# Optimization experiments

Measured on AMD Instinct MI355X. Metric: run time of the kernel, lower is better.

Reference implementation:

```python
import jax, jax.numpy as jnp
import numpy as np

NUM_HEADS = 16

def _stablemax3_s(x):
    # 3rd-order Taylor approx of exp(x), Eq 38
    pos = 1.0 + x * (1.0 + 0.5 * x * (1.0 + x / 3.0))
    neg = 1.0 / (1.0 - x * (1.0 - 0.5 * x * (1.0 - x / 3.0)))
    return jnp.where(x >= 0, pos, neg)

def stablemax3(logits, axis=-1):
    logits = logits - jnp.max(logits, axis=axis, keepdims=True)
    s = _stablemax3_s(logits)
    return s / jnp.sum(s, axis=axis, keepdims=True)

def setup_inputs() -> dict:
    key = jax.random.key(0)
    k1, k2, k3 = jax.random.split(key, 3)
    B, S, D = 2, 2048, 1024
    x = jax.random.normal(k1, (B, S, D), dtype=jnp.float32)
    w_qkv = jax.random.normal(k2, (3 * D, D), dtype=jnp.float32) * 0.02
    w_out = jax.random.normal(k3, (D, D), dtype=jnp.float32) * 0.02
    b_out = jnp.zeros((D,), dtype=jnp.float32)
    return {"x": x, "w_qkv": w_qkv, "w_out": w_out, "b_out": b_out}

def reference(x, w_qkv, w_out, b_out):
    B, S, D = x.shape
    H = NUM_HEADS
    hd = D // H
    scale = hd ** (-0.5)
    qkv = x @ w_qkv.T                                  # [B, S, 3D]
    qkv = qkv.reshape(B, S, 3, H, hd)
    qkv = jnp.transpose(qkv, (2, 0, 3, 1, 4))          # [3, B, H, S, hd]
    q, k, v = qkv[0], qkv[1], qkv[2]                   # pos(.) is identity here
    attn = jnp.einsum('bhsd,bhtd->bhst', q, k) * scale # [B, H, S, S]
    attn = stablemax3(attn, axis=-1)
    out = jnp.einsum('bhst,bhtd->bhsd', attn, v)       # [B, H, S, hd]
    out = jnp.transpose(out, (0, 2, 1, 3)).reshape(B, S, D)
    return out @ w_out.T + b_out
```

## Files before the change

### kernel.cpp

```cpp
#include <hip/hip_runtime.h>

typedef _Float16 half8 __attribute__((ext_vector_type(8)));
typedef _Float16 half4 __attribute__((ext_vector_type(4)));
typedef _Float16 half2v __attribute__((ext_vector_type(2)));
typedef float floatx4 __attribute__((ext_vector_type(4)));

__device__ __forceinline__ void gl_lds16(const _Float16* g, _Float16* l) {
    __builtin_amdgcn_global_load_lds(
        (const __attribute__((address_space(1))) void*)g,
        (__attribute__((address_space(3))) void*)l, 16, 0, 0);
}

__device__ __forceinline__ half2v cvt_pk(float a, float b) {
    return __builtin_bit_cast(half2v, __builtin_amdgcn_cvt_pkrtz(a, b));
}

__device__ __forceinline__ half2v rcp2(half2v d) {
#if __has_builtin(__builtin_amdgcn_rcph)
    half2v r;
    r[0] = __builtin_amdgcn_rcph(d[0]);
    r[1] = __builtin_amdgcn_rcph(d[1]);
    return r;
#else
    half2v r;
    r[0] = (_Float16)__builtin_amdgcn_rcpf((float)d[0]);
    r[1] = (_Float16)__builtin_amdgcn_rcpf((float)d[1]);
    return r;
#endif
}

__device__ __forceinline__ float dot2acc(half2v a, float acc) {
#if __has_builtin(__builtin_amdgcn_fdot2)
    const half2v one = {(_Float16)1.0f, (_Float16)1.0f};
    return __builtin_amdgcn_fdot2(a, one, acc, false);
#else
    return acc + (float)a[0] + (float)a[1];
#endif
}

__global__ __launch_bounds__(256) void cvt_f32_f16(const floatx4* __restrict__ in,
                                                   half4* __restrict__ out, int n4) {
    int i = blockIdx.x * 256 + threadIdx.x;
    if (i >= n4) return;
    floatx4 v = in[i];
    half4 h;
#pragma unroll
    for (int j = 0; j < 4; ++j) h[j] = (_Float16)v[j];
    out[i] = h;
}

__global__ __launch_bounds__(256) void gemm_qkv(const _Float16* __restrict__ A,
                                                const _Float16* __restrict__ B,
                                                _Float16* __restrict__ qh,
                                                _Float16* __restrict__ kh,
                                                _Float16* __restrict__ vth) {
    const int K = 1024;
    __shared__ _Float16 SH[128 * 68];
    _Float16* As = SH;
    _Float16* Bs = SH + 4096;
    const int t = threadIdx.x;
    const int lane = t & 63, w = t >> 6;
    const int l15 = lane & 15, quad = lane >> 4;
    const int wm = w >> 1, wn = w & 1;
    const int m0 = blockIdx.y * 128, n0 = blockIdx.x * 128;

    floatx4 acc[4][4];
    const floatx4 zf = {0.f, 0.f, 0.f, 0.f};
#pragma unroll
    for (int i = 0; i < 4; ++i)
#pragma unroll
        for (int j = 0; j < 4; ++j) acc[i][j] = zf;

    for (int kt = 0; kt < K; kt += 32) {
        __syncthreads();
#pragma unroll
        for (int it = 0; it < 2; ++it) {
            int cc = it * 256 + t;
            int row = cc >> 2, kc = cc & 3;
            gl_lds16(&A[(size_t)(m0 + row) * K + kt + kc * 8], &As[cc * 8]);
            gl_lds16(&B[(size_t)(n0 + row) * K + kt + kc * 8], &Bs[cc * 8]);
        }
        __syncthreads();
        half8 af[4], bfr[4];
#pragma unroll
        for (int i = 0; i < 4; ++i)
            af[i] = *(const half8*)&As[(wm * 64 + i * 16 + l15) * 32 + quad * 8];
#pragma unroll
        for (int i = 0; i < 4; ++i)
            bfr[i] = *(const half8*)&Bs[(wn * 64 + i * 16 + l15) * 32 + quad * 8];
#pragma unroll
        for (int mi = 0; mi < 4; ++mi)
#pragma unroll
            for (int ni = 0; ni < 4; ++ni)
                acc[mi][ni] = __builtin_amdgcn_mfma_f32_16x16x32_f16(af[mi], bfr[ni],
                                                                     acc[mi][ni], 0, 0, 0);
    }

    const int b = m0 >> 11, s0 = m0 & 2047;
#pragma unroll
    for (int hf = 0; hf < 2; ++hf) {
        __syncthreads();
        if (wn == hf) {
#pragma unroll
            for (int mi = 0; mi < 4; ++mi)
#pragma unroll
                for (int ni = 0; ni < 4; ++ni)
#pragma unroll
                    for (int r = 0; r < 4; ++r)
                        SH[(wm * 64 + mi * 16 + quad * 4 + r) * 68 + ni * 16 + l15] =
                            (_Float16)acc[mi][ni][r];
        }
        __syncthreads();
        const int cbase = n0 + hf * 64;
        if (n0 < 2048) {
            const int hh = (cbase & 1023) >> 6;
            _Float16* dst = (n0 < 1024 ? qh : kh) + (size_t)((b << 4) | hh) * 131072;
#pragma unroll
            for (int it = 0; it < 4; ++it) {
                int cc = it * 256 + t;
                int r = cc >> 3, c8 = cc & 7;
                half4 lo = *(const half4*)&SH[r * 68 + c8 * 8];
                half4 hi = *(const half4*)&SH[r * 68 + c8 * 8 + 4];
                half8 v;
#pragma unroll
                for (int j = 0; j < 4; ++j) { v[j] = lo[j]; v[j + 4] = hi[j]; }
                *(half8*)&dst[(size_t)(s0 + r) * 64 + c8 * 8] = v;
            }
        } else {
            const int hh = (cbase - 2048) >> 6;
            _Float16* dst = vth + (size_t)((b << 4) | hh) * 131072;
#pragma unroll
            for (int it = 0; it < 4; ++it) {
                int cc = it * 256 + t;
                int d = cc >> 4, s8 = cc & 15;
                half8 v;
#pragma unroll
                for (int j = 0; j < 8; ++j) v[j] = SH[(s8 * 8 + j) * 68 + d];
                *(half8*)&dst[(size_t)d * 2048 + s0 + s8 * 8] = v;
            }
        }
    }
}

__global__ __launch_bounds__(256) void gemm_out(const _Float16* __restrict__ A,
                                                const _Float16* __restrict__ B,
                                                float* __restrict__ C,
                                                const float* __restrict__ bias) {
    const int K = 1024, N = 1024;
    __shared__ _Float16 SH[6144];
    _Float16* As = SH;
    _Float16* Bs = SH + 2048;
    const int t = threadIdx.x;
    const int lane = t & 63, w = t >> 6;
    const int l15 = lane & 15, quad = lane >> 4;
    const int wm = w >> 1, wn = w & 1;
    const int m0 = blockIdx.y * 64, n0 = blockIdx.x * 128;

    floatx4 acc[2][4];
    const floatx4 zf = {0.f, 0.f, 0.f, 0.f};
#pragma unroll
    for (int i = 0; i < 2; ++i)
#pragma unroll
        for (int j = 0; j < 4; ++j) acc[i][j] = zf;

    for (int kt = 0; kt < K; kt += 32) {
        __syncthreads();
        {
            int row = t >> 2, kc = t & 3;
            gl_lds16(&A[(size_t)(m0 + row) * K + kt + kc * 8], &As[t * 8]);
        }
#pragma unroll
        for (int it = 0; it < 2; ++it) {
            int cc = it * 256 + t;
            int row = cc >> 2, kc = cc & 3;
            gl_lds16(&B[(size_t)(n0 + row) * K + kt + kc * 8], &Bs[cc * 8]);
        }
        __syncthreads();
        half8 af[2], bfr[4];
#pragma unroll
        for (int i = 0; i < 2; ++i)
            af[i] = *(const half8*)&As[(wm * 32 + i * 16 + l15) * 32 + quad * 8];
#pragma unroll
        for (int i = 0; i < 4; ++i)
            bfr[i] = *(const half8*)&Bs[(wn * 64 + i * 16 + l15) * 32 + quad * 8];
#pragma unroll
        for (int mi = 0; mi < 2; ++mi)
#pragma unroll
            for (int ni = 0; ni < 4; ++ni)
                acc[mi][ni] = __builtin_amdgcn_mfma_f32_16x16x32_f16(af[mi], bfr[ni],
                                                                     acc[mi][ni], 0, 0, 0);
    }

#pragma unroll
    for (int mi = 0; mi < 2; ++mi) {
#pragma unroll
        for (int ni = 0; ni < 4; ++ni) {
            int col = n0 + wn * 64 + ni * 16 + l15;
            float bv = bias[col];
#pragma unroll
            for (int r = 0; r < 4; ++r) {
                int row = m0 + wm * 32 + mi * 16 + quad * 4 + r;
                C[(size_t)row * N + col] = acc[mi][ni][r] + bv;
            }
        }
    }
}

__global__ __launch_bounds__(256) void attn_kernel(const _Float16* __restrict__ qh,
                                                   const _Float16* __restrict__ kh,
                                                   const _Float16* __restrict__ vth,
                                                   _Float16* __restrict__ out) {
    __shared__ _Float16 SM[2 * 64 * 72];
    _Float16* Ks = SM;
    _Float16* VTs = SM + 64 * 72;

    const int t = threadIdx.x;
    const int lane = t & 63, w = t >> 6;
    const int l15 = lane & 15, quad = lane >> 4;
    const int q0 = blockIdx.x * 128;
    const int bh = blockIdx.y;
    const int b = bh >> 4, h = bh & 15;

    const _Float16* Qp = qh + (size_t)bh * 131072 + q0 * 64;
    const _Float16* Kp = kh + (size_t)bh * 131072;
    const _Float16* VTp = vth + (size_t)bh * 131072;

    const floatx4 zf = {0.f, 0.f, 0.f, 0.f};

    half8 qf[2][2];
#pragma unroll
    for (int nh = 0; nh < 2; ++nh)
#pragma unroll
        for (int kk = 0; kk < 2; ++kk) {
            half8 q = *(const half8*)&Qp[(w * 32 + nh * 16 + l15) * 64 + kk * 32 + quad * 8];
#pragma unroll
            for (int j = 0; j < 8; ++j) q[j] = q[j] * (_Float16)0.125f;
            qf[nh][kk] = q;
        }

    float rmax[2] = {-1.0e30f, -1.0e30f};

    for (int kt = 0; kt < 2048; kt += 64) {
        __syncthreads();
#pragma unroll
        for (int it = 0; it < 2; ++it) {
            int cc = it * 256 + t;
            int r = cc >> 3, c8 = cc & 7;
            *(half8*)&Ks[r * 72 + c8 * 8] = *(const half8*)&Kp[kt * 64 + cc * 8];
        }
        __syncthreads();
        floatx4 sa[4][2];
#pragma unroll
        for (int T = 0; T < 4; ++T) { sa[T][0] = zf; sa[T][1] = zf; }
#pragma unroll
        for (int kk = 0; kk < 2; ++kk) {
            half8 kf[4];
#pragma unroll
            for (int T = 0; T < 4; ++T)
                kf[T] = *(const half8*)&Ks[(T * 16 + l15) * 72 + kk * 32 + quad * 8];
#pragma unroll
            for (int T = 0; T < 4; ++T)
#pragma unroll
                for (int nh = 0; nh < 2; ++nh)
                    sa[T][nh] = __builtin_amdgcn_mfma_f32_16x16x32_f16(kf[T], qf[nh][kk],
                                                                      sa[T][nh], 0, 0, 0);
        }
#pragma unroll
        for (int T = 0; T < 4; ++T)
#pragma unroll
            for (int nh = 0; nh < 2; ++nh)
#pragma unroll
                for (int r = 0; r < 4; ++r)
                    rmax[nh] = fmaxf(rmax[nh], sa[T][nh][r]);
    }
#pragma unroll
    for (int nh = 0; nh < 2; ++nh) {
        rmax[nh] = fmaxf(rmax[nh], __shfl_xor(rmax[nh], 16, 64));
        rmax[nh] = fmaxf(rmax[nh], __shfl_xor(rmax[nh], 32, 64));
    }
    const float xm[2] = {-rmax[0], -rmax[1]};

    const half2v cA = {(_Float16)(-1.0f / 6.0f), (_Float16)(-1.0f / 6.0f)};
    const half2v cB = {(_Float16)0.5f, (_Float16)0.5f};
    const half2v cC = {(_Float16)-1.0f, (_Float16)-1.0f};
    const half2v cD = {(_Float16)1.0f, (_Float16)1.0f};

    float rsum[2] = {0.f, 0.f};
    floatx4 oacc[4][2];
#pragma unroll
    for (int i = 0; i < 4; ++i) { oacc[i][0] = zf; oacc[i][1] = zf; }

    for (int kt = 0; kt < 2048; kt += 64) {
        __syncthreads();
#pragma unroll
        for (int it = 0; it < 2; ++it) {
            int cc = it * 256 + t;
            int r = cc >> 3, c8 = cc & 7;
            *(half8*)&Ks[r * 72 + c8 * 8] = *(const half8*)&Kp[kt * 64 + cc * 8];
            *(half8*)&VTs[r * 72 + c8 * 8] =
                *(const half8*)&VTp[(size_t)r * 2048 + kt + c8 * 8];
        }
        __syncthreads();
        floatx4 sa[4][2];
#pragma unroll
        for (int T = 0; T < 4; ++T) { sa[T][0] = zf; sa[T][1] = zf; }
#pragma unroll
        for (int kk = 0; kk < 2; ++kk) {
            half8 kf[4];
#pragma unroll
            for (int T = 0; T < 4; ++T)
                kf[T] = *(const half8*)&Ks[(T * 16 + l15) * 72 + kk * 32 + quad * 8];
#pragma unroll
            for (int T = 0; T < 4; ++T)
#pragma unroll
                for (int nh = 0; nh < 2; ++nh)
                    sa[T][nh] = __builtin_amdgcn_mfma_f32_16x16x32_f16(kf[T], qf[nh][kk],
                                                                      sa[T][nh], 0, 0, 0);
        }
#pragma unroll
        for (int c = 0; c < 2; ++c) {
            half8 vf[4];
#pragma unroll
            for (int di = 0; di < 4; ++di) {
                half4 lo = *(const half4*)&VTs[(di * 16 + l15) * 72 + c * 32 + 4 * quad];
                half4 hi = *(const half4*)&VTs[(di * 16 + l15) * 72 + c * 32 + 16 + 4 * quad];
                half8 vv;
#pragma unroll
                for (int j = 0; j < 4; ++j) { vv[j] = lo[j]; vv[j + 4] = hi[j]; }
                vf[di] = vv;
            }
#pragma unroll
            for (int nh = 0; nh < 2; ++nh) {
                half8 pb;
#pragma unroll
                for (int m = 0; m < 4; ++m) {
                    int T = 2 * c + (m >> 1);
                    int r0 = (m & 1) * 2;
                    half2v x2 = cvt_pk(sa[T][nh][r0] + xm[nh],
                                       sa[T][nh][r0 + 1] + xm[nh]);
                    half2v hp = __builtin_elementwise_fma(x2, cA, cB);
                    hp = __builtin_elementwise_fma(x2, hp, cC);
                    hp = __builtin_elementwise_fma(x2, hp, cD);
                    half2v p2 = rcp2(hp);
                    rsum[nh] = dot2acc(p2, rsum[nh]);
                    pb[2 * m] = p2[0];
                    pb[2 * m + 1] = p2[1];
                }
#pragma unroll
                for (int di = 0; di < 4; ++di)
                    oacc[di][nh] = __builtin_amdgcn_mfma_f32_16x16x32_f16(vf[di], pb,
                                                                         oacc[di][nh], 0, 0, 0);
            }
        }
    }

#pragma unroll
    for (int nh = 0; nh < 2; ++nh) {
        rsum[nh] += __shfl_xor(rsum[nh], 16, 64);
        rsum[nh] += __shfl_xor(rsum[nh], 32, 64);
    }
    const float inv[2] = {1.0f / rsum[0], 1.0f / rsum[1]};

    __syncthreads();
    _Float16* Os = SM;
#pragma unroll
    for (int di = 0; di < 4; ++di) {
#pragma unroll
        for (int nh = 0; nh < 2; ++nh) {
            half4 hv;
#pragma unroll
            for (int r = 0; r < 4; ++r) hv[r] = (_Float16)(oacc[di][nh][r] * inv[nh]);
            *(half4*)&Os[(w * 32 + nh * 16 + l15) * 72 + di * 16 + quad * 4] = hv;
        }
    }
    __syncthreads();
    _Float16* Op = out + (size_t)(b * 2048 + q0) * 1024 + h * 64;
#pragma unroll
    for (int it = 0; it < 4; ++it) {
        int cc = it * 256 + t;
        int r = cc >> 3, c8 = cc & 7;
        *(half8*)&Op[(size_t)r * 1024 + c8 * 8] = *(const half8*)&Os[r * 72 + c8 * 8];
    }
}

extern "C" void kernel_launch(void* const* d_in, const int* in_sizes, int n_in,
                              void* d_out, int out_size, void* d_ws, size_t ws_size,
                              hipStream_t stream) {
    const float* x_f = (const float*)d_in[0];
    const float* wqkv_f = (const float*)d_in[1];
    const float* wout_f = (const float*)d_in[2];
    const float* bias_f = (const float*)d_in[3];

    char* ws = (char*)d_ws;
    _Float16* xh = (_Float16*)(ws);
    _Float16* aoh = xh;
    _Float16* wqh = (_Float16*)(ws + 8388608);
    _Float16* woh = wqh;
    _Float16* qh = (_Float16*)(ws + 14680064);
    _Float16* kh = (_Float16*)(ws + 23068672);
    _Float16* vth = (_Float16*)(ws + 31457280);

    cvt_f32_f16<<<4096, 256, 0, stream>>>((const floatx4*)x_f, (half4*)xh, 1048576);
    cvt_f32_f16<<<3072, 256, 0, stream>>>((const floatx4*)wqkv_f, (half4*)wqh, 786432);
    gemm_qkv<<<dim3(24, 32), 256, 0, stream>>>(xh, wqh, qh, kh, vth);
    cvt_f32_f16<<<1024, 256, 0, stream>>>((const floatx4*)wout_f, (half4*)woh, 262144);
    attn_kernel<<<dim3(16, 32), 256, 0, stream>>>(qh, kh, vth, aoh);
    gemm_out<<<dim3(8, 64), 256, 0, stream>>>(aoh, woh, (float*)d_out, bias_f);
}
```

Baseline: 216.8 us.

## Double-buffer K/V tiles in LDS with register prefetch in attention loops

Both attention passes now prefetch the next K (and V^T) tile into registers while computing on the current one. The prefetched tile is written into an alternate LDS buffer, which drops one __syncthreads per iteration. The aim is to hide global load latency behind MFMA work. In exchange it doubles LDS use to four buffers and raises register pressure, which could lower occupancy.

New measurement: 216.0 us. No clear change (-0.3%).

```diff
diff --git a/kernel.cpp b/kernel.cpp
--- a/kernel.cpp
+++ b/kernel.cpp
@@ -210,9 +210,7 @@
                                                    const _Float16* __restrict__ kh,
                                                    const _Float16* __restrict__ vth,
                                                    _Float16* __restrict__ out) {
-    __shared__ _Float16 SM[2 * 64 * 72];
-    _Float16* Ks = SM;
-    _Float16* VTs = SM + 64 * 72;
+    __shared__ _Float16 SM[4 * 4608];
 
     const int t = threadIdx.x;
     const int lane = t & 63, w = t >> 6;
@@ -227,6 +225,10 @@
 
     const floatx4 zf = {0.f, 0.f, 0.f, 0.f};
 
+    const int cc0 = t, cc1 = 256 + t;
+    const int kr0 = cc0 >> 3, kc0 = (cc0 & 7) * 8;
+    const int kr1 = cc1 >> 3, kc1 = (cc1 & 7) * 8;
+
     half8 qf[2][2];
 #pragma unroll
     for (int nh = 0; nh < 2; ++nh)
@@ -239,16 +241,22 @@
         }
 
     float rmax[2] = {-1.0e30f, -1.0e30f};
+    half8 kreg0, kreg1;
+
+    kreg0 = *(const half8*)&Kp[cc0 * 8];
+    kreg1 = *(const half8*)&Kp[cc1 * 8];
+    *(half8*)&SM[kr0 * 72 + kc0] = kreg0;
+    *(half8*)&SM[kr1 * 72 + kc1] = kreg1;
 
     for (int kt = 0; kt < 2048; kt += 64) {
         __syncthreads();
-#pragma unroll
-        for (int it = 0; it < 2; ++it) {
-            int cc = it * 256 + t;
-            int r = cc >> 3, c8 = cc & 7;
-            *(half8*)&Ks[r * 72 + c8 * 8] = *(const half8*)&Kp[kt * 64 + cc * 8];
-        }
-        __syncthreads();
+        const int cur = (kt >> 6) & 1;
+        const _Float16* Ks = SM + cur * 4608;
+        const bool more = kt + 64 < 2048;
+        if (more) {
+            kreg0 = *(const half8*)&Kp[(kt + 64) * 64 + cc0 * 8];
+            kreg1 = *(const half8*)&Kp[(kt + 64) * 64 + cc1 * 8];
+        }
         floatx4 sa[4][2];
 #pragma unroll
         for (int T = 0; T < 4; ++T) { sa[T][0] = zf; sa[T][1] = zf; }
@@ -272,6 +280,11 @@
 #pragma unroll
                 for (int r = 0; r < 4; ++r)
                     rmax[nh] = fmaxf(rmax[nh], sa[T][nh][r]);
+        if (more) {
+            _Float16* Kn = SM + (cur ^ 1) * 4608;
+            *(half8*)&Kn[kr0 * 72 + kc0] = kreg0;
+            *(half8*)&Kn[kr1 * 72 + kc1] = kreg1;
+        }
     }
 #pragma unroll
     for (int nh = 0; nh < 2; ++nh) {
@@ -290,17 +303,29 @@
 #pragma unroll
     for (int i = 0; i < 4; ++i) { oacc[i][0] = zf; oacc[i][1] = zf; }
 
+    half8 vreg0, vreg1;
+    kreg0 = *(const half8*)&Kp[cc0 * 8];
+    kreg1 = *(const half8*)&Kp[cc1 * 8];
+    vreg0 = *(const half8*)&VTp[(size_t)kr0 * 2048 + kc0];
+    vreg1 = *(const half8*)&VTp[(size_t)kr1 * 2048 + kc1];
+    __syncthreads();
+    *(half8*)&SM[kr0 * 72 + kc0] = kreg0;
+    *(half8*)&SM[kr1 * 72 + kc1] = kreg1;
+    *(half8*)&SM[2 * 4608 + kr0 * 72 + kc0] = vreg0;
+    *(half8*)&SM[2 * 4608 + kr1 * 72 + kc1] = vreg1;
+
     for (int kt = 0; kt < 2048; kt += 64) {
         __syncthreads();
-#pragma unroll
-        for (int it = 0; it < 2; ++it) {
-            int cc = it * 256 + t;
-            int r = cc >> 3, c8 = cc & 7;
-            *(half8*)&Ks[r * 72 + c8 * 8] = *(const half8*)&Kp[kt * 64 + cc * 8];
-            *(half8*)&VTs[r * 72 + c8 * 8] =
-                *(const half8*)&VTp[(size_t)r * 2048 + kt + c8 * 8];
-        }
-        __syncthreads();
+        const int cur = (kt >> 6) & 1;
+        const _Float16* Ks = SM + cur * 4608;
+        const _Float16* VTs = SM + (2 + cur) * 4608;
+        const bool more = kt + 64 < 2048;
+        if (more) {
+            kreg0 = *(const half8*)&Kp[(kt + 64) * 64 + cc0 * 8];
+            kreg1 = *(const half8*)&Kp[(kt + 64) * 64 + cc1 * 8];
+            vreg0 = *(const half8*)&VTp[(size_t)kr0 * 2048 + (kt + 64) + kc0];
+            vreg1 = *(const half8*)&VTp[(size_t)kr1 * 2048 + (kt + 64) + kc1];
+        }
         floatx4 sa[4][2];
 #pragma unroll
         for (int T = 0; T < 4; ++T) { sa[T][0] = zf; sa[T][1] = zf; }
@@ -352,6 +377,14 @@
                                                                          oacc[di][nh], 0, 0, 0);
             }
         }
+        if (more) {
+            _Float16* Kn = SM + (cur ^ 1) * 4608;
+            _Float16* Vn = SM + (2 + (cur ^ 1)) * 4608;
+            *(half8*)&Kn[kr0 * 72 + kc0] = kreg0;
+            *(half8*)&Kn[kr1 * 72 + kc1] = kreg1;
+            *(half8*)&Vn[kr0 * 72 + kc0] = vreg0;
+            *(half8*)&Vn[kr1 * 72 + kc1] = vreg1;
+        }
     }
 
 #pragma unroll
```

## Halve attention query tile to 64 rows and merge input conversion kernels

Applied to the files above, without the earlier changes.

The attention kernel now gives each block 64 query rows instead of 128, one 16-row strip per wave. This doubles the grid to 1024 blocks so the GPU is better filled and register pressure drops. The cost is twice the K/V loading from global memory and LDS per query row, and half the MFMA work per K/V tile. Separately, the conversions of x and w_qkv are fused into one launch to save a kernel launch.

Result: slower. 249.4 us (+15.1%).

```diff
diff --git a/kernel.cpp b/kernel.cpp
--- a/kernel.cpp
+++ b/kernel.cpp
@@ -36,6 +36,27 @@
 #else
     return acc + (float)a[0] + (float)a[1];
 #endif
+}
+
+__global__ __launch_bounds__(256) void cvt_xw(const floatx4* __restrict__ x,
+                                              const floatx4* __restrict__ wq,
+                                              half4* __restrict__ xh,
+                                              half4* __restrict__ wqh) {
+    int i = blockIdx.x * 256 + threadIdx.x;
+    floatx4 v;
+    half4 h;
+    if (i < 1048576) {
+        v = x[i];
+#pragma unroll
+        for (int j = 0; j < 4; ++j) h[j] = (_Float16)v[j];
+        xh[i] = h;
+    } else {
+        int j4 = i - 1048576;
+        v = wq[j4];
+#pragma unroll
+        for (int j = 0; j < 4; ++j) h[j] = (_Float16)v[j];
+        wqh[j4] = h;
+    }
 }
 
 __global__ __launch_bounds__(256) void cvt_f32_f16(const floatx4* __restrict__ in,
@@ -217,7 +238,7 @@
     const int t = threadIdx.x;
     const int lane = t & 63, w = t >> 6;
     const int l15 = lane & 15, quad = lane >> 4;
-    const int q0 = blockIdx.x * 128;
+    const int q0 = blockIdx.x * 64;
     const int bh = blockIdx.y;
     const int b = bh >> 4, h = bh & 15;
 
@@ -226,19 +247,18 @@
     const _Float16* VTp = vth + (size_t)bh * 131072;
 
     const floatx4 zf = {0.f, 0.f, 0.f, 0.f};
-
-    half8 qf[2][2];
-#pragma unroll
-    for (int nh = 0; nh < 2; ++nh)
-#pragma unroll
-        for (int kk = 0; kk < 2; ++kk) {
-            half8 q = *(const half8*)&Qp[(w * 32 + nh * 16 + l15) * 64 + kk * 32 + quad * 8];
-#pragma unroll
-            for (int j = 0; j < 8; ++j) q[j] = q[j] * (_Float16)0.125f;
-            qf[nh][kk] = q;
-        }
-
-    float rmax[2] = {-1.0e30f, -1.0e30f};
+    const int qrow = w * 16 + l15;
+
+    half8 qf[2];
+#pragma unroll
+    for (int kk = 0; kk < 2; ++kk) {
+        half8 q = *(const half8*)&Qp[qrow * 64 + kk * 32 + quad * 8];
+#pragma unroll
+        for (int j = 0; j < 8; ++j) q[j] = q[j] * (_Float16)0.125f;
+        qf[kk] = q;
+    }
+
+    float rmax = -1.0e30f;
 
     for (int kt = 0; kt < 2048; kt += 64) {
         __syncthreads();
@@ -249,9 +269,9 @@
             *(half8*)&Ks[r * 72 + c8 * 8] = *(const half8*)&Kp[kt * 64 + cc * 8];
         }
         __syncthreads();
-        floatx4 sa[4][2];
-#pragma unroll
-        for (int T = 0; T < 4; ++T) { sa[T][0] = zf; sa[T][1] = zf; }
+        floatx4 sa[4];
+#pragma unroll
+        for (int T = 0; T < 4; ++T) sa[T] = zf;
 #pragma unroll
         for (int kk = 0; kk < 2; ++kk) {
             half8 kf[4];
@@ -260,35 +280,27 @@
                 kf[T] = *(const half8*)&Ks[(T * 16 + l15) * 72 + kk * 32 + quad * 8];
 #pragma unroll
             for (int T = 0; T < 4; ++T)
-#pragma unroll
-                for (int nh = 0; nh < 2; ++nh)
-                    sa[T][nh] = __builtin_amdgcn_mfma_f32_16x16x32_f16(kf[T], qf[nh][kk],
-                                                                      sa[T][nh], 0, 0, 0);
+                sa[T] = __builtin_amdgcn_mfma_f32_16x16x32_f16(kf[T], qf[kk], sa[T], 0, 0, 0);
         }
 #pragma unroll
         for (int T = 0; T < 4; ++T)
 #pragma unroll
-            for (int nh = 0; nh < 2; ++nh)
-#pragma unroll
-                for (int r = 0; r < 4; ++r)
-                    rmax[nh] = fmaxf(rmax[nh], sa[T][nh][r]);
-    }
-#pragma unroll
-    for (int nh = 0; nh < 2; ++nh) {
-        rmax[nh] = fmaxf(rmax[nh], __shfl_xor(rmax[nh], 16, 64));
-        rmax[nh] = fmaxf(rmax[nh], __shfl_xor(rmax[nh], 32, 64));
-    }
-    const float xm[2] = {-rmax[0], -rmax[1]};
+            for (int r = 0; r < 4; ++r)
+                rmax = fmaxf(rmax, sa[T][r]);
+    }
+    rmax = fmaxf(rmax, __shfl_xor(rmax, 16, 64));
+    rmax = fmaxf(rmax, __shfl_xor(rmax, 32, 64));
+    const float xm = -rmax;
 
     const half2v cA = {(_Float16)(-1.0f / 6.0f), (_Float16)(-1.0f / 6.0f)};
     const half2v cB = {(_Float16)0.5f, (_Float16)0.5f};
     const half2v cC = {(_Float16)-1.0f, (_Float16)-1.0f};
     const half2v cD = {(_Float16)1.0f, (_Float16)1.0f};
 
-    float rsum[2] = {0.f, 0.f};
-    floatx4 oacc[4][2];
-#pragma unroll
-    for (int i = 0; i < 4; ++i) { oacc[i][0] = zf; oacc[i][1] = zf; }
+    float rsum = 0.f;
+    floatx4 oacc[4];
+#pragma unroll
+    for (int i = 0; i < 4; ++i) oacc[i] = zf;
 
     for (int kt = 0; kt < 2048; kt += 64) {
         __syncthreads();
@@ -301,9 +313,9 @@
                 *(const half8*)&VTp[(size_t)r * 2048 + kt + c8 * 8];
         }
         __syncthreads();
-        floatx4 sa[4][2];
-#pragma unroll
-        for (int T = 0; T < 4; ++T) { sa[T][0] = zf; sa[T][1] = zf; }
+        floatx4 sa[4];
+#pragma unroll
+        for (int T = 0; T < 4; ++T) sa[T] = zf;
 #pragma unroll
         for (int kk = 0; kk < 2; ++kk) {
             half8 kf[4];
@@ -312,10 +324,7 @@
                 kf[T] = *(const half8*)&Ks[(T * 16 + l15) * 72 + kk * 32 + quad * 8];
 #pragma unroll
             for (int T = 0; T < 4; ++T)
-#pragma unroll
-                for (int nh = 0; nh < 2; ++nh)
-                    sa[T][nh] = __builtin_amdgcn_mfma_f32_16x16x32_f16(kf[T], qf[nh][kk],
-                                                                      sa[T][nh], 0, 0, 0);
+                sa[T] = __builtin_amdgcn_mfma_f32_16x16x32_f16(kf[T], qf[kk], sa[T], 0, 0, 0);
         }
 #pragma unroll
         for (int c = 0; c < 2; ++c) {
@@ -329,54 +338,44 @@
                 for (int j = 0; j < 4; ++j) { vv[j] = lo[j]; vv[j + 4] = hi[j]; }
                 vf[di] = vv;
             }
-#pragma unroll
-            for (int nh = 0; nh < 2; ++nh) {
-                half8 pb;
-#pragma unroll
-                for (int m = 0; m < 4; ++m) {
-                    int T = 2 * c + (m >> 1);
-                    int r0 = (m & 1) * 2;
-                    half2v x2 = cvt_pk(sa[T][nh][r0] + xm[nh],
-                                       sa[T][nh][r0 + 1] + xm[nh]);
-                    half2v hp = __builtin_elementwise_fma(x2, cA, cB);
-                    hp = __builtin_elementwise_fma(x2, hp, cC);
-                    hp = __builtin_elementwise_fma(x2, hp, cD);
-                    half2v p2 = rcp2(hp);
-                    rsum[nh] = dot2acc(p2, rsum[nh]);
-                    pb[2 * m] = p2[0];
-                    pb[2 * m + 1] = p2[1];
-                }
-#pragma unroll
-                for (int di = 0; di < 4; ++di)
-                    oacc[di][nh] = __builtin_amdgcn_mfma_f32_16x16x32_f16(vf[di], pb,
-                                                                         oacc[di][nh], 0, 0, 0);
+            half8 pb;
+#pragma unroll
+            for (int m = 0; m < 4; ++m) {
+                int T = 2 * c + (m >> 1);
+                int r0 = (m & 1) * 2;
+                half2v x2 = cvt_pk(sa[T][r0] + xm, sa[T][r0 + 1] + xm);
+                half2v hp = __builtin_elementwise_fma(x2, cA, cB);
+                hp = __builtin_elementwise_fma(x2, hp, cC);
+                hp = __builtin_elementwise_fma(x2, hp, cD);
+                half2v p2 = rcp2(hp);
+                rsum = dot2acc(p2, rsum);
+                pb[2 * m] = p2[0];
+                pb[2 * m + 1] = p2[1];
             }
-        }
-    }
-
-#pragma unroll
-    for (int nh = 0; nh < 2; ++nh) {
-        rsum[nh] += __shfl_xor(rsum[nh], 16, 64);
-        rsum[nh] += __shfl_xor(rsum[nh], 32, 64);
-    }
-    const float inv[2] = {1.0f / rsum[0], 1.0f / rsum[1]};
+#pragma unroll
+            for (int di = 0; di < 4; ++di)
+                oacc[di] = __builtin_amdgcn_mfma_f32_16x16x32_f16(vf[di], pb,
+                                                                 oacc[di], 0, 0, 0);
+        }
+    }
+
+    rsum += __shfl_xor(rsum, 16, 64);
+    rsum += __shfl_xor(rsum, 32, 64);
+    const float inv = 1.0f / rsum;
 
     __syncthreads();
     _Float16* Os = SM;
 #pragma unroll
     for (int di = 0; di < 4; ++di) {
-#pragma unroll
-        for (int nh = 0; nh < 2; ++nh) {
-            half4 hv;
-#pragma unroll
-            for (int r = 0; r < 4; ++r) hv[r] = (_Float16)(oacc[di][nh][r] * inv[nh]);
-            *(half4*)&Os[(w * 32 + nh * 16 + l15) * 72 + di * 16 + quad * 4] = hv;
-        }
+        half4 hv;
+#pragma unroll
+        for (int r = 0; r < 4; ++r) hv[r] = (_Float16)(oacc[di][r] * inv);
+        *(half4*)&Os[qrow * 72 + di * 16 + quad * 4] = hv;
     }
     __syncthreads();
     _Float16* Op = out + (size_t)(b * 2048 + q0) * 1024 + h * 64;
 #pragma unroll
-    for (int it = 0; it < 4; ++it) {
+    for (int it = 0; it < 2; ++it) {
         int cc = it * 256 + t;
         int r = cc >> 3, c8 = cc & 7;
         *(half8*)&Op[(size_t)r * 1024 + c8 * 8] = *(const half8*)&Os[r * 72 + c8 * 8];
@@ -400,10 +399,10 @@
     _Float16* kh = (_Float16*)(ws + 23068672);
     _Float16* vth = (_Float16*)(ws + 31457280);
 
-    cvt_f32_f16<<<4096, 256, 0, stream>>>((const floatx4*)x_f, (half4*)xh, 1048576);
-    cvt_f32_f16<<<3072, 256, 0, stream>>>((const floatx4*)wqkv_f, (half4*)wqh, 786432);
+    cvt_xw<<<7168, 256, 0, stream>>>((const floatx4*)x_f, (const floatx4*)wqkv_f,
+                                     (half4*)xh, (half4*)wqh);
     gemm_qkv<<<dim3(24, 32), 256, 0, stream>>>(xh, wqh, qh, kh, vth);
     cvt_f32_f16<<<1024, 256, 0, stream>>>((const floatx4*)wout_f, (half4*)woh, 262144);
-    attn_kernel<<<dim3(16, 32), 256, 0, stream>>>(qh, kh, vth, aoh);
+    attn_kernel<<<dim3(32, 32), 256, 0, stream>>>(qh, kh, vth, aoh);
     gemm_out<<<dim3(8, 64), 256, 0, stream>>>(aoh, woh, (float*)d_out, bias_f);
 }
```

## Double attention key tile to 128 and merge input conversion kernels

Applied to the files above, without the earlier changes.

The attention kernel now stages 128 keys per iteration instead of 64 in both the max pass and the accumulation pass. This halves the number of barrier-separated load phases, and the score MFMAs are reorganised so only two key subtiles are live at a time. The LDS footprint grows to about 35 KB, which may lower occupancy. Separately, the x and w_qkv fp32-to-fp16 conversions are fused into one launch to save launch overhead.

Measured after the change: 240.9 us. +11.1%, slower.

```diff
diff --git a/kernel.cpp b/kernel.cpp
--- a/kernel.cpp
+++ b/kernel.cpp
@@ -36,6 +36,27 @@
 #else
     return acc + (float)a[0] + (float)a[1];
 #endif
+}
+
+__global__ __launch_bounds__(256) void cvt_xw(const floatx4* __restrict__ x,
+                                              const floatx4* __restrict__ wq,
+                                              half4* __restrict__ xh,
+                                              half4* __restrict__ wqh) {
+    int i = blockIdx.x * 256 + threadIdx.x;
+    floatx4 v;
+    half4 h;
+    if (i < 1048576) {
+        v = x[i];
+#pragma unroll
+        for (int j = 0; j < 4; ++j) h[j] = (_Float16)v[j];
+        xh[i] = h;
+    } else {
+        int j4 = i - 1048576;
+        v = wq[j4];
+#pragma unroll
+        for (int j = 0; j < 4; ++j) h[j] = (_Float16)v[j];
+        wqh[j4] = h;
+    }
 }
 
 __global__ __launch_bounds__(256) void cvt_f32_f16(const floatx4* __restrict__ in,
@@ -210,9 +231,9 @@
                                                    const _Float16* __restrict__ kh,
                                                    const _Float16* __restrict__ vth,
                                                    _Float16* __restrict__ out) {
-    __shared__ _Float16 SM[2 * 64 * 72];
+    __shared__ _Float16 SM[128 * 72 + 64 * 136];
     _Float16* Ks = SM;
-    _Float16* VTs = SM + 64 * 72;
+    _Float16* VTs = SM + 128 * 72;
 
     const int t = threadIdx.x;
     const int lane = t & 63, w = t >> 6;
@@ -240,38 +261,29 @@
 
     float rmax[2] = {-1.0e30f, -1.0e30f};
 
-    for (int kt = 0; kt < 2048; kt += 64) {
-        __syncthreads();
-#pragma unroll
-        for (int it = 0; it < 2; ++it) {
+    for (int kt = 0; kt < 2048; kt += 128) {
+        __syncthreads();
+#pragma unroll
+        for (int it = 0; it < 4; ++it) {
             int cc = it * 256 + t;
             int r = cc >> 3, c8 = cc & 7;
-            *(half8*)&Ks[r * 72 + c8 * 8] = *(const half8*)&Kp[kt * 64 + cc * 8];
-        }
-        __syncthreads();
-        floatx4 sa[4][2];
-#pragma unroll
-        for (int T = 0; T < 4; ++T) { sa[T][0] = zf; sa[T][1] = zf; }
-#pragma unroll
-        for (int kk = 0; kk < 2; ++kk) {
-            half8 kf[4];
-#pragma unroll
-            for (int T = 0; T < 4; ++T)
-                kf[T] = *(const half8*)&Ks[(T * 16 + l15) * 72 + kk * 32 + quad * 8];
-#pragma unroll
-            for (int T = 0; T < 4; ++T)
-#pragma unroll
-                for (int nh = 0; nh < 2; ++nh)
-                    sa[T][nh] = __builtin_amdgcn_mfma_f32_16x16x32_f16(kf[T], qf[nh][kk],
-                                                                      sa[T][nh], 0, 0, 0);
-        }
-#pragma unroll
-        for (int T = 0; T < 4; ++T)
-#pragma unroll
-            for (int nh = 0; nh < 2; ++nh)
-#pragma unroll
-                for (int r = 0; r < 4; ++r)
-                    rmax[nh] = fmaxf(rmax[nh], sa[T][nh][r]);
+            *(half8*)&Ks[r * 72 + c8 * 8] = *(const half8*)&Kp[(size_t)(kt + r) * 64 + c8 * 8];
+        }
+        __syncthreads();
+#pragma unroll
+        for (int T = 0; T < 8; ++T) {
+            half8 kf0 = *(const half8*)&Ks[(T * 16 + l15) * 72 + quad * 8];
+            half8 kf1 = *(const half8*)&Ks[(T * 16 + l15) * 72 + 32 + quad * 8];
+            floatx4 sa0 = __builtin_amdgcn_mfma_f32_16x16x32_f16(kf0, qf[0][0], zf, 0, 0, 0);
+            sa0 = __builtin_amdgcn_mfma_f32_16x16x32_f16(kf1, qf[0][1], sa0, 0, 0, 0);
+            floatx4 sa1 = __builtin_amdgcn_mfma_f32_16x16x32_f16(kf0, qf[1][0], zf, 0, 0, 0);
+            sa1 = __builtin_amdgcn_mfma_f32_16x16x32_f16(kf1, qf[1][1], sa1, 0, 0, 0);
+#pragma unroll
+            for (int r = 0; r < 4; ++r) {
+                rmax[0] = fmaxf(rmax[0], sa0[r]);
+                rmax[1] = fmaxf(rmax[1], sa1[r]);
+            }
+        }
     }
 #pragma unroll
     for (int nh = 0; nh < 2; ++nh) {
@@ -290,40 +302,37 @@
 #pragma unroll
     for (int i = 0; i < 4; ++i) { oacc[i][0] = zf; oacc[i][1] = zf; }
 
-    for (int kt = 0; kt < 2048; kt += 64) {
-        __syncthreads();
-#pragma unroll
-        for (int it = 0; it < 2; ++it) {
+    for (int kt = 0; kt < 2048; kt += 128) {
+        __syncthreads();
+#pragma unroll
+        for (int it = 0; it < 4; ++it) {
             int cc = it * 256 + t;
             int r = cc >> 3, c8 = cc & 7;
-            *(half8*)&Ks[r * 72 + c8 * 8] = *(const half8*)&Kp[kt * 64 + cc * 8];
-            *(half8*)&VTs[r * 72 + c8 * 8] =
-                *(const half8*)&VTp[(size_t)r * 2048 + kt + c8 * 8];
-        }
-        __syncthreads();
-        floatx4 sa[4][2];
-#pragma unroll
-        for (int T = 0; T < 4; ++T) { sa[T][0] = zf; sa[T][1] = zf; }
-#pragma unroll
-        for (int kk = 0; kk < 2; ++kk) {
-            half8 kf[4];
-#pragma unroll
-            for (int T = 0; T < 4; ++T)
-                kf[T] = *(const half8*)&Ks[(T * 16 + l15) * 72 + kk * 32 + quad * 8];
-#pragma unroll
-            for (int T = 0; T < 4; ++T)
-#pragma unroll
-                for (int nh = 0; nh < 2; ++nh)
-                    sa[T][nh] = __builtin_amdgcn_mfma_f32_16x16x32_f16(kf[T], qf[nh][kk],
-                                                                      sa[T][nh], 0, 0, 0);
-        }
-#pragma unroll
-        for (int c = 0; c < 2; ++c) {
+            *(half8*)&Ks[r * 72 + c8 * 8] = *(const half8*)&Kp[(size_t)(kt + r) * 64 + c8 * 8];
+            int d = cc >> 4, k8 = cc & 15;
+            *(half8*)&VTs[d * 136 + k8 * 8] =
+                *(const half8*)&VTp[(size_t)d * 2048 + kt + k8 * 8];
+        }
+        __syncthreads();
+#pragma unroll
+        for (int c = 0; c < 4; ++c) {
+            half8 kfa0 = *(const half8*)&Ks[((2 * c) * 16 + l15) * 72 + quad * 8];
+            half8 kfa1 = *(const half8*)&Ks[((2 * c) * 16 + l15) * 72 + 32 + quad * 8];
+            half8 kfb0 = *(const half8*)&Ks[((2 * c + 1) * 16 + l15) * 72 + quad * 8];
+            half8 kfb1 = *(const half8*)&Ks[((2 * c + 1) * 16 + l15) * 72 + 32 + quad * 8];
+            floatx4 sa[2][2];
+#pragma unroll
+            for (int nh = 0; nh < 2; ++nh) {
+                sa[0][nh] = __builtin_amdgcn_mfma_f32_16x16x32_f16(kfa0, qf[nh][0], zf, 0, 0, 0);
+                sa[0][nh] = __builtin_amdgcn_mfma_f32_16x16x32_f16(kfa1, qf[nh][1], sa[0][nh], 0, 0, 0);
+                sa[1][nh] = __builtin_amdgcn_mfma_f32_16x16x32_f16(kfb0, qf[nh][0], zf, 0, 0, 0);
+                sa[1][nh] = __builtin_amdgcn_mfma_f32_16x16x32_f16(kfb1, qf[nh][1], sa[1][nh], 0, 0, 0);
+            }
             half8 vf[4];
 #pragma unroll
             for (int di = 0; di < 4; ++di) {
-                half4 lo = *(const half4*)&VTs[(di * 16 + l15) * 72 + c * 32 + 4 * quad];
-                half4 hi = *(const half4*)&VTs[(di * 16 + l15) * 72 + c * 32 + 16 + 4 * quad];
+                half4 lo = *(const half4*)&VTs[(di * 16 + l15) * 136 + c * 32 + 4 * quad];
+                half4 hi = *(const half4*)&VTs[(di * 16 + l15) * 136 + c * 32 + 16 + 4 * quad];
                 half8 vv;
 #pragma unroll
                 for (int j = 0; j < 4; ++j) { vv[j] = lo[j]; vv[j + 4] = hi[j]; }
@@ -334,10 +343,10 @@
                 half8 pb;
 #pragma unroll
                 for (int m = 0; m < 4; ++m) {
-                    int T = 2 * c + (m >> 1);
+                    int Tl = m >> 1;
                     int r0 = (m & 1) * 2;
-                    half2v x2 = cvt_pk(sa[T][nh][r0] + xm[nh],
-                                       sa[T][nh][r0 + 1] + xm[nh]);
+                    half2v x2 = cvt_pk(sa[Tl][nh][r0] + xm[nh],
+                                       sa[Tl][nh][r0 + 1] + xm[nh]);
                     half2v hp = __builtin_elementwise_fma(x2, cA, cB);
                     hp = __builtin_elementwise_fma(x2, hp, cC);
                     hp = __builtin_elementwise_fma(x2, hp, cD);
@@ -400,8 +409,8 @@
     _Float16* kh = (_Float16*)(ws + 23068672);
     _Float16* vth = (_Float16*)(ws + 31457280);
 
-    cvt_f32_f16<<<4096, 256, 0, stream>>>((const floatx4*)x_f, (half4*)xh, 1048576);
-    cvt_f32_f16<<<3072, 256, 0, stream>>>((const floatx4*)wqkv_f, (half4*)wqh, 786432);
+    cvt_xw<<<7168, 256, 0, stream>>>((const floatx4*)x_f, (const floatx4*)wqkv_f,
+                                     (half4*)xh, (half4*)wqh);
     gemm_qkv<<<dim3(24, 32), 256, 0, stream>>>(xh, wqh, qh, kh, vth);
     cvt_f32_f16<<<1024, 256, 0, stream>>>((const floatx4*)wout_f, (half4*)woh, 262144);
     attn_kernel<<<dim3(16, 32), 256, 0, stream>>>(qh, kh, vth, aoh);
```
